# Kernel optimization log

Hardware: AMD Instinct MI355X
Metric: run time of the kernel (lower is better)

## Reference

```python
import jax, jax.numpy as jnp
import numpy as np


def setup_inputs() -> dict:
    key = jax.random.key(0)
    k1, k2 = jax.random.split(key)
    B, C, H, W, F = 32, 256, 64, 64, 256
    inputs = jax.random.normal(k1, (B, C, H, W), dtype=jnp.float32)
    biases = jax.random.normal(k2, (1, 1, C, F), dtype=jnp.float32)
    return {"inputs": inputs, "biases": biases}


def _mix_weights(biases):
    # UnitSphereInit.get_log_prob: unit-sphere parameterization of a
    # probability vector over input channels: p_cf = b_cf^2 / sum_c b_cf^2.
    # The original computes log(p) and later exponentiates inside logsumexp;
    # we keep p directly (same math, fewer transcendentals).
    sq = biases * biases                      # (1,1,C,F)
    p = sq / jnp.sum(sq, axis=2, keepdims=True)
    return p.reshape(biases.shape[2], biases.shape[3])  # (C, F)


def reference(inputs, biases):
    # out[b,f,h,w] = logsumexp_c( x[b,c,h,w] + log p[c,f] )
    #             = m[b,h,w] + log( sum_c exp(x - m) * p[c,f] )
    # p <= 1 so the exp is safe; the channel reduction over all filters
    # fuses into one GEMM (single pass over the input, all filters at once).
    p = _mix_weights(biases)                          # (C, F)
    m = jnp.max(inputs, axis=1, keepdims=True)        # (B,1,H,W)
    e = jnp.exp(inputs - m)                           # (B,C,H,W)
    s = jnp.einsum('bchw,cf->bfhw', e, p)             # (B,F,H,W)
    return m + jnp.log(s)
```

## Files before the change

### kernel.cpp

```cpp
#include <hip/hip_runtime.h>
#include <stdint.h>

#define C_DIM  256
#define F_DIM  256
#define HW     4096
#define TW     128
#define NCHUNK 8
#define ETP    40

typedef __attribute__((ext_vector_type(8))) short   bf16x8;
typedef __attribute__((ext_vector_type(4))) float   floatx4;

__device__ __forceinline__ unsigned short f32_to_bf16(float f) {
    union { float f; unsigned int u; } v; v.f = f;
    unsigned int u = v.u;
    return (unsigned short)((u + 0x7FFFu + ((u >> 16) & 1u)) >> 16);
}

__device__ __forceinline__ void async_load16(const float* g, float* l) {
    __builtin_amdgcn_global_load_lds(
        (const __attribute__((address_space(1))) void*)g,
        (__attribute__((address_space(3))) void*)l, 16, 0, 0);
}

__global__ void prep_kernel(const float* __restrict__ b,
                            unsigned short* __restrict__ apack) {
    __shared__ float part[16][17];
    __shared__ float inv_s[16];
    const int t     = threadIdx.x;
    const int ftile = blockIdx.x;
    const int f0    = ftile * 16;

    const int fl = t & 15;
    const int cg = t >> 4;
    float s = 0.f;
#pragma unroll
    for (int k = 0; k < 16; ++k) {
        float v = b[(cg + 16 * k) * F_DIM + f0 + fl];
        s += v * v;
    }
    part[cg][fl] = s;
    __syncthreads();
    if (t < 16) {
        float acc = 0.f;
#pragma unroll
        for (int g = 0; g < 16; ++g) acc += part[g][t];
        inv_s[t] = 1.0f / acc;
    }
    __syncthreads();

#pragma unroll
    for (int e = t; e < 512; e += 256) {
        const int kiter = e >> 6;
        const int lane  = e & 63;
        const int f     = f0 + (lane & 15);
        const int c0    = kiter * 32 + ((lane >> 4) << 3);
        const float inv = inv_s[lane & 15];
        bf16x8 v;
#pragma unroll
        for (int i = 0; i < 8; ++i) {
            float w = b[(c0 + i) * F_DIM + f];
            v[i] = (short)f32_to_bf16(w * w * inv);
        }
        *(bf16x8*)(apack + ((size_t)(ftile * 8 + kiter) * 64 + lane) * 8) = v;
    }
}

__global__ __launch_bounds__(512, 4)
void mixture_kernel(const float* __restrict__ x,
                    const unsigned short* __restrict__ apack,
                    float* __restrict__ out) {
    __shared__ __align__(16) float          sbuf[2][32][TW];
    __shared__ __align__(16) unsigned short et[2][TW][ETP];

    const int t     = threadIdx.x;
    const int wv    = t >> 6;
    const int lane  = t & 63;
    const int batch = blockIdx.x >> 5;
    const int hw0   = (blockIdx.x & 31) * TW;

    const float* xb = x + (size_t)batch * C_DIM * HW + hw0;

#define DMA_CHUNK(ck, buf)                                                      \
    {                                                                           \
        _Pragma("unroll")                                                       \
        for (int r = 0; r < 2; ++r) {                                           \
            const int rr = 4 * wv + 2 * r;                                      \
            const float* g = xb + (size_t)((ck) * 32 + rr + (lane >> 5)) * HW   \
                                + (lane & 31) * 4;                              \
            async_load16(g, &sbuf[buf][rr][0]);                                 \
        }                                                                       \
    }

    const int llo = lane & 15;
    const int lhi = lane >> 4;
    const int j   = t & 127;
    const int cg  = t >> 7;

    floatx4 acc[2][8];
#pragma unroll
    for (int a = 0; a < 2; ++a)
#pragma unroll
        for (int jt = 0; jt < 8; ++jt)
            acc[a][jt] = (floatx4){0.f, 0.f, 0.f, 0.f};

    const bf16x8* ap = (const bf16x8*)apack;

    DMA_CHUNK(0, 0);

#pragma unroll
    for (int i = 0; i < NCHUNK; ++i) {
        const int b = i & 1;

        bf16x8 afrag0 = ap[((2 * wv + 0) * 8 + i) * 64 + lane];
        bf16x8 afrag1 = ap[((2 * wv + 1) * 8 + i) * 64 + lane];

        if (i < NCHUNK - 1) {
            DMA_CHUNK(i + 1, b ^ 1);
            asm volatile("s_waitcnt vmcnt(2)\n\ts_barrier" ::: "memory");
        } else {
            asm volatile("s_waitcnt vmcnt(0)\n\ts_barrier" ::: "memory");
        }

        {
            float xv[8];
#pragma unroll
            for (int q = 0; q < 8; ++q) xv[q] = sbuf[b][cg * 8 + q][j];
            bf16x8 v;
#pragma unroll
            for (int q = 0; q < 8; ++q) v[q] = (short)f32_to_bf16(__expf(xv[q]));
            *(bf16x8*)&et[b][j][cg * 8] = v;
        }
        asm volatile("s_waitcnt lgkmcnt(0)\n\ts_barrier" ::: "memory");

#pragma unroll
        for (int jt = 0; jt < 8; ++jt) {
            bf16x8 bfrag = *(const bf16x8*)&et[b][jt * 16 + llo][lhi * 8];
            acc[0][jt] = __builtin_amdgcn_mfma_f32_16x16x32_bf16(
                afrag0, bfrag, acc[0][jt], 0, 0, 0);
            acc[1][jt] = __builtin_amdgcn_mfma_f32_16x16x32_bf16(
                afrag1, bfrag, acc[1][jt], 0, 0, 0);
        }
    }

    float* ob = out + (size_t)batch * F_DIM * HW + hw0;
#pragma unroll
    for (int a = 0; a < 2; ++a) {
        const int fbase = 32 * wv + 16 * a + lhi * 4;
#pragma unroll
        for (int r = 0; r < 4; ++r) {
            float* orow = ob + (size_t)(fbase + r) * HW;
#pragma unroll
            for (int jt = 0; jt < 8; ++jt)
                orow[jt * 16 + llo] = __logf(acc[a][jt][r]);
        }
    }
}

extern "C" void kernel_launch(void* const* d_in, const int* in_sizes, int n_in,
                              void* d_out, int out_size, void* d_ws, size_t ws_size,
                              hipStream_t stream) {
    const float* x      = (const float*)d_in[0];
    const float* biases = (const float*)d_in[1];
    float* out = (float*)d_out;

    unsigned short* apack = (unsigned short*)d_ws;

    prep_kernel<<<16, 256, 0, stream>>>(biases, apack);
    mixture_kernel<<<1024, 512, 0, stream>>>(x, apack, out);
}
```

Before: 242.8 us.

## Triple-buffer input chunks and software-pipeline exp-transpose behind MFMA

Grows the LDS staging buffer to three chunks so the DMA runs two chunks ahead. The exp/bf16 transpose of the next chunk now happens right after the current chunk's MFMAs, and the weight fragments are prefetched one iteration early. This merges the two barriers per iteration into one, meant to hide global-load latency and overlap transcendental work with matrix work. The extra LDS (about 68KB per block) may cut the number of resident blocks per CU and so reduce occupancy.

```diff
diff --git a/kernel.cpp b/kernel.cpp
--- a/kernel.cpp
+++ b/kernel.cpp
@@ -70,7 +70,7 @@
 void mixture_kernel(const float* __restrict__ x,
                     const unsigned short* __restrict__ apack,
                     float* __restrict__ out) {
-    __shared__ __align__(16) float          sbuf[2][32][TW];
+    __shared__ __align__(16) float          sbuf[3][32][TW];
     __shared__ __align__(16) unsigned short et[2][TW][ETP];
 
     const int t     = threadIdx.x;
@@ -92,6 +92,17 @@
         }                                                                       \
     }
 
+#define TRANSPOSE_CHUNK(sb, eb)                                                 \
+    {                                                                           \
+        float xv[8];                                                            \
+        _Pragma("unroll")                                                       \
+        for (int q = 0; q < 8; ++q) xv[q] = sbuf[sb][cg * 8 + q][j];            \
+        bf16x8 v;                                                               \
+        _Pragma("unroll")                                                       \
+        for (int q = 0; q < 8; ++q) v[q] = (short)f32_to_bf16(__expf(xv[q]));   \
+        *(bf16x8*)&et[eb][j][cg * 8] = v;                                       \
+    }
+
     const int llo = lane & 15;
     const int lhi = lane >> 4;
     const int j   = t & 127;
@@ -107,40 +118,43 @@
     const bf16x8* ap = (const bf16x8*)apack;
 
     DMA_CHUNK(0, 0);
+    asm volatile("" ::: "memory");
+    bf16x8 a0c = ap[((2 * wv + 0) * 8 + 0) * 64 + lane];
+    bf16x8 a1c = ap[((2 * wv + 1) * 8 + 0) * 64 + lane];
+    DMA_CHUNK(1, 1);
+    asm volatile("s_waitcnt vmcnt(4)\n\ts_barrier" ::: "memory");
+    TRANSPOSE_CHUNK(0, 0);
 
 #pragma unroll
     for (int i = 0; i < NCHUNK; ++i) {
-        const int b = i & 1;
+        const int eb = i & 1;
 
-        bf16x8 afrag0 = ap[((2 * wv + 0) * 8 + i) * 64 + lane];
-        bf16x8 afrag1 = ap[((2 * wv + 1) * 8 + i) * 64 + lane];
+        bf16x8 a0n, a1n;
+        if (i < NCHUNK - 1) {
+            a0n = ap[((2 * wv + 0) * 8 + (i + 1)) * 64 + lane];
+            a1n = ap[((2 * wv + 1) * 8 + (i + 1)) * 64 + lane];
+        }
+        if (i < NCHUNK - 2) DMA_CHUNK(i + 2, (i + 2) % 3);
 
-        if (i < NCHUNK - 1) {
-            DMA_CHUNK(i + 1, b ^ 1);
-            asm volatile("s_waitcnt vmcnt(2)\n\ts_barrier" ::: "memory");
-        } else {
-            asm volatile("s_waitcnt vmcnt(0)\n\ts_barrier" ::: "memory");
-        }
-
-        {
-            float xv[8];
-#pragma unroll
-            for (int q = 0; q < 8; ++q) xv[q] = sbuf[b][cg * 8 + q][j];
-            bf16x8 v;
-#pragma unroll
-            for (int q = 0; q < 8; ++q) v[q] = (short)f32_to_bf16(__expf(xv[q]));
-            *(bf16x8*)&et[b][j][cg * 8] = v;
-        }
-        asm volatile("s_waitcnt lgkmcnt(0)\n\ts_barrier" ::: "memory");
+        if (i < NCHUNK - 2)
+            asm volatile("s_waitcnt vmcnt(4) lgkmcnt(0)\n\ts_barrier" ::: "memory");
+        else if (i == NCHUNK - 2)
+            asm volatile("s_waitcnt vmcnt(2) lgkmcnt(0)\n\ts_barrier" ::: "memory");
+        else
+            asm volatile("s_waitcnt vmcnt(0) lgkmcnt(0)\n\ts_barrier" ::: "memory");
 
 #pragma unroll
         for (int jt = 0; jt < 8; ++jt) {
-            bf16x8 bfrag = *(const bf16x8*)&et[b][jt * 16 + llo][lhi * 8];
+            bf16x8 bfrag = *(const bf16x8*)&et[eb][jt * 16 + llo][lhi * 8];
             acc[0][jt] = __builtin_amdgcn_mfma_f32_16x16x32_bf16(
-                afrag0, bfrag, acc[0][jt], 0, 0, 0);
+                a0c, bfrag, acc[0][jt], 0, 0, 0);
             acc[1][jt] = __builtin_amdgcn_mfma_f32_16x16x32_bf16(
-                afrag1, bfrag, acc[1][jt], 0, 0, 0);
+                a1c, bfrag, acc[1][jt], 0, 0, 0);
         }
+
+        if (i < NCHUNK - 1) TRANSPOSE_CHUNK((i + 1) % 3, eb ^ 1);
+
+        if (i < NCHUNK - 1) { a0c = a0n; a1c = a1n; }
     }
 
     float* ob = out + (size_t)batch * F_DIM * HW + hw0;
```

New measurement: 243.1 us, median of 2. No clear change (+0.1%).

## Load inputs directly into MFMA B-fragments in registers, dropping LDS staging

Applied to the files above, without the earlier changes.

Replaces the LDS-staged async DMA plus exp/transpose pass with per-lane global loads. Each lane fetches exactly the eight channel values it needs for its B-fragment, computes exp and bf16 packing in registers, and prefetches the next chunk into registers. Blocks shrink to 256 threads covering 64 spatial positions, so the grid doubles, and each wave now covers 8 filter tiles by 2 position tiles. This removes the LDS traffic and barriers, at the cost of strided 4-byte global loads (16 contiguous floats per row segment) and more A-fragment loads from global memory per block.

```diff
diff --git a/kernel.cpp b/kernel.cpp
--- a/kernel.cpp
+++ b/kernel.cpp
@@ -4,9 +4,8 @@
 #define C_DIM  256
 #define F_DIM  256
 #define HW     4096
-#define TW     128
+#define JT     64
 #define NCHUNK 8
-#define ETP    40
 
 typedef __attribute__((ext_vector_type(8))) short   bf16x8;
 typedef __attribute__((ext_vector_type(4))) float   floatx4;
@@ -15,12 +14,6 @@
     union { float f; unsigned int u; } v; v.f = f;
     unsigned int u = v.u;
     return (unsigned short)((u + 0x7FFFu + ((u >> 16) & 1u)) >> 16);
-}
-
-__device__ __forceinline__ void async_load16(const float* g, float* l) {
-    __builtin_amdgcn_global_load_lds(
-        (const __attribute__((address_space(1))) void*)g,
-        (__attribute__((address_space(3))) void*)l, 16, 0, 0);
 }
 
 __global__ void prep_kernel(const float* __restrict__ b,
@@ -66,93 +59,85 @@
     }
 }
 
-__global__ __launch_bounds__(512, 4)
+__global__ __launch_bounds__(256, 4)
 void mixture_kernel(const float* __restrict__ x,
                     const unsigned short* __restrict__ apack,
                     float* __restrict__ out) {
-    __shared__ __align__(16) float          sbuf[2][32][TW];
-    __shared__ __align__(16) unsigned short et[2][TW][ETP];
-
     const int t     = threadIdx.x;
     const int wv    = t >> 6;
     const int lane  = t & 63;
-    const int batch = blockIdx.x >> 5;
-    const int hw0   = (blockIdx.x & 31) * TW;
+    const int llo   = lane & 15;
+    const int lhi   = lane >> 4;
+    const int fg    = wv & 1;
+    const int jg    = wv >> 1;
+    const int batch = blockIdx.x >> 6;
+    const int hw0   = (blockIdx.x & 63) * JT;
 
-    const float* xb = x + (size_t)batch * C_DIM * HW + hw0;
-
-#define DMA_CHUNK(ck, buf)                                                      \
-    {                                                                           \
-        _Pragma("unroll")                                                       \
-        for (int r = 0; r < 2; ++r) {                                           \
-            const int rr = 4 * wv + 2 * r;                                      \
-            const float* g = xb + (size_t)((ck) * 32 + rr + (lane >> 5)) * HW   \
-                                + (lane & 31) * 4;                              \
-            async_load16(g, &sbuf[buf][rr][0]);                                 \
-        }                                                                       \
-    }
-
-    const int llo = lane & 15;
-    const int lhi = lane >> 4;
-    const int j   = t & 127;
-    const int cg  = t >> 7;
-
-    floatx4 acc[2][8];
-#pragma unroll
-    for (int a = 0; a < 2; ++a)
-#pragma unroll
-        for (int jt = 0; jt < 8; ++jt)
-            acc[a][jt] = (floatx4){0.f, 0.f, 0.f, 0.f};
+    const float* xl = x + (size_t)batch * C_DIM * HW
+                        + (size_t)(lhi * 8) * HW + hw0 + jg * 32 + llo;
 
     const bf16x8* ap = (const bf16x8*)apack;
 
-    DMA_CHUNK(0, 0);
+    floatx4 acc[8][2];
+#pragma unroll
+    for (int ft = 0; ft < 8; ++ft)
+#pragma unroll
+        for (int jj = 0; jj < 2; ++jj)
+            acc[ft][jj] = (floatx4){0.f, 0.f, 0.f, 0.f};
+
+    float xc[2][8];
+#pragma unroll
+    for (int jj = 0; jj < 2; ++jj)
+#pragma unroll
+        for (int q = 0; q < 8; ++q)
+            xc[jj][q] = xl[(size_t)q * HW + jj * 16];
 
 #pragma unroll
-    for (int i = 0; i < NCHUNK; ++i) {
-        const int b = i & 1;
-
-        bf16x8 afrag0 = ap[((2 * wv + 0) * 8 + i) * 64 + lane];
-        bf16x8 afrag1 = ap[((2 * wv + 1) * 8 + i) * 64 + lane];
-
-        if (i < NCHUNK - 1) {
-            DMA_CHUNK(i + 1, b ^ 1);
-            asm volatile("s_waitcnt vmcnt(2)\n\ts_barrier" ::: "memory");
-        } else {
-            asm volatile("s_waitcnt vmcnt(0)\n\ts_barrier" ::: "memory");
+    for (int ck = 0; ck < NCHUNK; ++ck) {
+        float xn[2][8];
+        if (ck < NCHUNK - 1) {
+#pragma unroll
+            for (int jj = 0; jj < 2; ++jj)
+#pragma unroll
+                for (int q = 0; q < 8; ++q)
+                    xn[jj][q] = xl[(size_t)((ck + 1) * 32 + q) * HW + jj * 16];
         }
 
-        {
-            float xv[8];
+        bf16x8 bfr[2];
 #pragma unroll
-            for (int q = 0; q < 8; ++q) xv[q] = sbuf[b][cg * 8 + q][j];
-            bf16x8 v;
+        for (int jj = 0; jj < 2; ++jj)
 #pragma unroll
-            for (int q = 0; q < 8; ++q) v[q] = (short)f32_to_bf16(__expf(xv[q]));
-            *(bf16x8*)&et[b][j][cg * 8] = v;
-        }
-        asm volatile("s_waitcnt lgkmcnt(0)\n\ts_barrier" ::: "memory");
+            for (int q = 0; q < 8; ++q)
+                bfr[jj][q] = (short)f32_to_bf16(__expf(xc[jj][q]));
 
 #pragma unroll
-        for (int jt = 0; jt < 8; ++jt) {
-            bf16x8 bfrag = *(const bf16x8*)&et[b][jt * 16 + llo][lhi * 8];
-            acc[0][jt] = __builtin_amdgcn_mfma_f32_16x16x32_bf16(
-                afrag0, bfrag, acc[0][jt], 0, 0, 0);
-            acc[1][jt] = __builtin_amdgcn_mfma_f32_16x16x32_bf16(
-                afrag1, bfrag, acc[1][jt], 0, 0, 0);
+        for (int ft = 0; ft < 8; ++ft) {
+            bf16x8 af = ap[((size_t)(fg * 8 + ft) * 8 + ck) * 64 + lane];
+            acc[ft][0] = __builtin_amdgcn_mfma_f32_16x16x32_bf16(
+                af, bfr[0], acc[ft][0], 0, 0, 0);
+            acc[ft][1] = __builtin_amdgcn_mfma_f32_16x16x32_bf16(
+                af, bfr[1], acc[ft][1], 0, 0, 0);
+        }
+
+        if (ck < NCHUNK - 1) {
+#pragma unroll
+            for (int jj = 0; jj < 2; ++jj)
+#pragma unroll
+                for (int q = 0; q < 8; ++q)
+                    xc[jj][q] = xn[jj][q];
         }
     }
 
-    float* ob = out + (size_t)batch * F_DIM * HW + hw0;
+    float* ob = out + (size_t)batch * F_DIM * HW + hw0 + jg * 32 + llo;
 #pragma unroll
-    for (int a = 0; a < 2; ++a) {
-        const int fbase = 32 * wv + 16 * a + lhi * 4;
+    for (int ft = 0; ft < 8; ++ft) {
+        const int fbase = (fg * 8 + ft) * 16 + lhi * 4;
 #pragma unroll
         for (int r = 0; r < 4; ++r) {
             float* orow = ob + (size_t)(fbase + r) * HW;
 #pragma unroll
-            for (int jt = 0; jt < 8; ++jt)
-                orow[jt * 16 + llo] = __logf(acc[a][jt][r]);
+            for (int jj = 0; jj < 2; ++jj)
+                orow[jj * 16] = __logf(acc[ft][jj][r]);
         }
     }
 }
@@ -167,5 +152,5 @@
     unsigned short* apack = (unsigned short*)d_ws;
 
     prep_kernel<<<16, 256, 0, stream>>>(biases, apack);
-    mixture_kernel<<<1024, 512, 0, stream>>>(x, apack, out);
+    mixture_kernel<<<2048, 256, 0, stream>>>(x, apack, out);
 }
```

New measurement: 291.5 us. 20.1% more time.
